# Kernel tuning notes

Measured on AMD Instinct MI355X. Metric: run time of the kernel, lower is better.

## Reference

```python
import jax, jax.numpy as jnp
import numpy as np

B, S, D = 1, 65536, 1024
NH = 8
HD = D // NH
M = 8          # memory_tokens
HID = 2048     # d_model * mlp_ratio(2.0)
EPS_LN = 1e-5
EPS_L = 1e-9


def setup_inputs() -> dict:
    key = jax.random.key(0)
    ks = jax.random.split(key, 16)
    def w(k, shape, s=0.02):
        return jax.random.normal(k, shape, dtype=jnp.float32) * s
    return {
        "h_img_seq": jax.random.normal(ks[0], (B, S, D), dtype=jnp.float32),
        "latents": w(ks[1], (M, D)),
        "wq": w(ks[2], (D, D)), "bq": jnp.zeros((D,), jnp.float32),
        "wk": w(ks[3], (D, D)), "bk": jnp.zeros((D,), jnp.float32),
        "wv": w(ks[4], (D, D)), "bv": jnp.zeros((D,), jnp.float32),
        "wo": w(ks[5], (D, D)), "bo": jnp.zeros((D,), jnp.float32),
        "ln_g": jnp.ones((D,), jnp.float32), "ln_b": jnp.zeros((D,), jnp.float32),
        "w1": w(ks[6], (D, HID)), "b1": jnp.zeros((HID,), jnp.float32),
        "w2": w(ks[7], (HID, D)), "b2": jnp.zeros((D,), jnp.float32),
    }


def reference(h_img_seq, latents, wq, bq, wk, bk, wv, bv, wo, bo,
              ln_g, ln_b, w1, b1, w2, b2):
    b, s, d = h_img_seq.shape
    scale = HD ** -0.5
    # queries from latents: [M, NH, HD] (shared across batch)
    q = (latents @ wq + bq).reshape(M, NH, HD).astype(jnp.float32)
    # K/V projections over the long sequence: [B, S, NH, HD] (fp32 accum)
    k = (h_img_seq @ wk + bk).reshape(b, s, NH, HD).astype(jnp.float32)
    v = (h_img_seq @ wv + bv).reshape(b, s, NH, HD).astype(jnp.float32)
    # online-softmax over chunks == stable softmax over full S (denominator l + 1e-9)
    logits = jnp.einsum('mhd,bshd->bhms', q, k) * scale          # [B, NH, M, S]
    mmax = jnp.max(logits, axis=-1, keepdims=True)
    e = jnp.exp(logits - mmax)
    l = jnp.sum(e, axis=-1, keepdims=True)                       # [B, NH, M, 1]
    acc = jnp.einsum('bhms,bshd->bhmd', e, v)                    # [B, NH, M, HD]
    out = acc / (l + EPS_L)
    out = out.transpose(0, 2, 1, 3).reshape(b, M, d).astype(h_img_seq.dtype)
    out = out @ wo + bo
    # MLP: LayerNorm -> Linear -> GELU(exact) -> Linear, residual
    mu = jnp.mean(out, axis=-1, keepdims=True)
    var = jnp.mean((out - mu) ** 2, axis=-1, keepdims=True)
    h = (out - mu) * jax.lax.rsqrt(var + EPS_LN) * ln_g + ln_b
    h = jax.nn.gelu(h @ w1 + b1, approximate=False) @ w2 + b2
    out = out + h
    m_vec = out.mean(axis=1)
    return (out, m_vec)
```

## Files before the change

### kernel.cpp

```cpp
#include <hip/hip_runtime.h>
#include <stdint.h>
#include <math.h>

#define S_LEN   65536
#define DM      1024
#define HD_     128
#define HID_    2048
#define SCALE_F 0.08838834764831845f

typedef float          f32x4  __attribute__((ext_vector_type(4)));
typedef short          bf16x8 __attribute__((ext_vector_type(8)));
typedef unsigned short u16;

__device__ __forceinline__ u16 f2bf(float f) {
  union { float f; uint32_t u; } v; v.f = f;
  uint32_t u = v.u;
  u += 0x7FFFu + ((u >> 16) & 1u);
  return (u16)(u >> 16);
}

__device__ __forceinline__ bf16x8 pack_bf8(const float* f) {
  union { bf16x8 v; u16 s[8]; } r;
#pragma unroll
  for (int i = 0; i < 8; ++i) r.s[i] = f2bf(f[i]);
  return r.v;
}

#define WS_Q      0u
#define WS_QKA    32768u
#define WS_QBK    163840u
#define WS_LSUM   164352u
#define WS_PLSUM  164608u
#define WS_XN     167936u
#define WS_EWH    430080u
#define WS_PMAX   698368u
#define WS_OATT   960512u
#define WS_O2     993280u
#define WS_H1     1026048u
#define WS_PBASE  2097152u
#define WS_LOGITS 2097152u
#define WS_PEW    2097152u
#define WS_E      34603008u

template<int KS>
__global__ __launch_bounds__(256) void k_sk8(const float* __restrict__ X,
                                             const float* __restrict__ W,
                                             float* __restrict__ P,
                                             int C, int K, int ncg) {
  int cg = blockIdx.x % ncg, kb = blockIdx.x / ncg;
  int c = (cg << 9) + threadIdx.x * 2;
  int k0 = kb * KS;
  float2 acc[8];
#pragma unroll
  for (int r = 0; r < 8; ++r) { acc[r].x = 0.f; acc[r].y = 0.f; }
  const float* wp = W + (size_t)k0 * C + c;
#pragma unroll 8
  for (int i = 0; i < KS; ++i) {
    float2 w = *(const float2*)wp; wp += C;
#pragma unroll
    for (int r = 0; r < 8; ++r) {
      float xv = X[r * K + k0 + i];
      acc[r].x += xv * w.x; acc[r].y += xv * w.y;
    }
  }
  float* pp = P + (size_t)(kb * 8) * C + c;
#pragma unroll
  for (int r = 0; r < 8; ++r) *(float2*)(pp + (size_t)r * C) = acc[r];
}

__global__ __launch_bounds__(256) void k_sk8h(const float* __restrict__ ewh,
                                              const float* __restrict__ wv,
                                              float* __restrict__ Pa) {
  int h = blockIdx.x & 7, kb = blockIdx.x >> 3;
  int lane = threadIdx.x & 63, q4 = threadIdx.x >> 6;
  int c = h * 128 + lane * 2;
  int k0 = kb * 64 + q4 * 16;
  const float* xp = ewh + h * 8192 + k0 * 8;
  const float* wp = wv + (size_t)k0 * 1024 + c;
  float2 acc[8];
#pragma unroll
  for (int m = 0; m < 8; ++m) { acc[m].x = 0.f; acc[m].y = 0.f; }
#pragma unroll
  for (int i = 0; i < 16; ++i) {
    float2 w = *(const float2*)wp; wp += 1024;
#pragma unroll
    for (int m = 0; m < 8; ++m) {
      float xv = xp[i * 8 + m];
      acc[m].x += xv * w.x; acc[m].y += xv * w.y;
    }
  }
  int slab = kb * 4 + q4;
  float* pp = Pa + (size_t)(slab * 8) * 1024 + c;
#pragma unroll
  for (int m = 0; m < 8; ++m) *(float2*)(pp + (size_t)m * 1024) = acc[m];
}

__global__ void k_red_q(const float* __restrict__ P, const float* __restrict__ bq,
                        float* __restrict__ q) {
  int idx = blockIdx.x * 256 + threadIdx.x;
  int m = idx >> 10, c = idx & 1023;
  float s = bq[c];
#pragma unroll 8
  for (int ks = 0; ks < 32; ++ks) s += P[(size_t)(ks * 8 + m) * 1024 + c];
  q[idx] = s;
}

__global__ __launch_bounds__(256) void k_foldqk(const float* __restrict__ q,
                                                const float* __restrict__ wk,
                                                const float* __restrict__ bk,
                                                u16* __restrict__ qka,
                                                float* __restrict__ qbk) {
  __shared__ float tile[64 * 129];
  int h = blockIdx.x & 7, ib = blockIdx.x >> 3;
  int i0 = ib * 64;
  int t = threadIdx.x;
  if (ib == 0 && t < 64) {
    int m = t >> 3, part = t & 7;
    float s = 0.f;
#pragma unroll
    for (int d = 0; d < 16; ++d)
      s += q[m * 1024 + h * 128 + part * 16 + d] * bk[h * 128 + part * 16 + d];
    s += __shfl_xor(s, 1);
    s += __shfl_xor(s, 2);
    s += __shfl_xor(s, 4);
    if (part == 0) qbk[m * 8 + h] = s * SCALE_F;
  }
  {
    int ii = t >> 2, dg = (t & 3) * 32;
    const float* src = wk + (size_t)(i0 + ii) * 1024 + h * 128 + dg;
    float* dst = tile + ii * 129 + dg;
#pragma unroll
    for (int u = 0; u < 8; ++u) {
      f32x4 v = *(const f32x4*)(src + u * 4);
      dst[u * 4 + 0] = v[0]; dst[u * 4 + 1] = v[1];
      dst[u * 4 + 2] = v[2]; dst[u * 4 + 3] = v[3];
    }
  }
  __syncthreads();
  int ii = t & 63, q4 = t >> 6;
  int i = i0 + ii;
  float a0 = 0.f, a1 = 0.f;
#pragma unroll 16
  for (int d = 0; d < 128; ++d) {
    float w = tile[ii * 129 + d];
    a0 += q[(q4 * 2 + 0) * 1024 + h * 128 + d] * w;
    a1 += q[(q4 * 2 + 1) * 1024 + h * 128 + d] * w;
  }
#pragma unroll
  for (int j = 0; j < 2; ++j) {
    int m = q4 * 2 + j;
    int r = m * 8 + h;
    float val = (j == 0 ? a0 : a1) * SCALE_F;
    int K0 = i >> 5, rb = r >> 4, hi = (i & 31) >> 3, e = i & 7, l16 = r & 15;
    int lane = hi * 16 + l16;
    qka[(((K0 * 4 + rb) * 64 + lane) << 3) + e] = f2bf(val);
  }
}

__global__ __launch_bounds__(256) void k_logits(
    const float* __restrict__ h, const u16* __restrict__ qka,
    const float* __restrict__ qbk, float* __restrict__ logits,
    float* __restrict__ pmax) {
  __shared__ float pmL[4 * 64];
  int t = threadIdx.x, wg = blockIdx.x;
  int w = t >> 6, l = t & 63;
  int g = l >> 4, l15 = l & 15;
  int scol = wg * 64 + w * 16 + l15;
  const bf16x8* qf = (const bf16x8*)qka;

  f32x4 acc[4];
#pragma unroll
  for (int rb = 0; rb < 4; ++rb) acc[rb] = (f32x4){0.f, 0.f, 0.f, 0.f};

#pragma unroll 2
  for (int ks = 0; ks < 32; ++ks) {
    const float* hp = h + (size_t)scol * DM + ks * 32 + g * 8;
    float fb[8];
    f32x4 f0 = *(const f32x4*)hp;
    f32x4 f1 = *(const f32x4*)(hp + 4);
    fb[0]=f0[0]; fb[1]=f0[1]; fb[2]=f0[2]; fb[3]=f0[3];
    fb[4]=f1[0]; fb[5]=f1[1]; fb[6]=f1[2]; fb[7]=f1[3];
    bf16x8 bfr = pack_bf8(fb);
#pragma unroll
    for (int rb = 0; rb < 4; ++rb) {
      bf16x8 af = qf[(ks * 4 + rb) * 64 + l];
      acc[rb] = __builtin_amdgcn_mfma_f32_16x16x32_bf16(af, bfr, acc[rb], 0, 0, 0);
    }
  }

#pragma unroll
  for (int rb = 0; rb < 4; ++rb) {
#pragma unroll
    for (int j = 0; j < 4; ++j) {
      int r = rb * 16 + g * 4 + j;
      float val = acc[rb][j] + qbk[r];
      logits[(size_t)r * S_LEN + scol] = val;
      float mx = val;
      mx = fmaxf(mx, __shfl_xor(mx, 1));
      mx = fmaxf(mx, __shfl_xor(mx, 2));
      mx = fmaxf(mx, __shfl_xor(mx, 4));
      mx = fmaxf(mx, __shfl_xor(mx, 8));
      if (l15 == 0) pmL[w * 64 + r] = mx;
    }
  }
  __syncthreads();
  if (t < 64) {
    float m0 = fmaxf(fmaxf(pmL[t], pmL[64 + t]), fmaxf(pmL[128 + t], pmL[192 + t]));
    pmax[(size_t)t * 1024 + wg] = m0;
  }
}

__global__ void k_make_e(const float* __restrict__ logits, const float* __restrict__ pmax,
                         u16* __restrict__ E, float* __restrict__ plsum) {
  int b = blockIdx.x, t = threadIdx.x;
  int r = b >> 3, sc = b & 7;
  __shared__ float red[256];
  float mv = -3.0e38f;
#pragma unroll
  for (int i = 0; i < 4; ++i) mv = fmaxf(mv, pmax[(size_t)r * 1024 + t + i * 256]);
  red[t] = mv; __syncthreads();
  for (int s = 128; s > 0; s >>= 1) {
    if (t < s) red[t] = fmaxf(red[t], red[t + s]);
    __syncthreads();
  }
  float gm = red[0];
  __syncthreads();

  size_t base = (size_t)r * S_LEN + sc * 8192 + t * 32;
  const float* lp = logits + base;
  u16* ep = E + base;
  float sum = 0.f;
#pragma unroll
  for (int gi = 0; gi < 4; ++gi) {
    f32x4 f0 = *(const f32x4*)(lp + gi * 8);
    f32x4 f1 = *(const f32x4*)(lp + gi * 8 + 4);
    float e[8];
#pragma unroll
    for (int i = 0; i < 4; ++i) { e[i] = expf(f0[i] - gm); e[4 + i] = expf(f1[i] - gm); }
    union { uint4 u4; u16 s[8]; } pk;
#pragma unroll
    for (int i = 0; i < 8; ++i) { sum += e[i]; pk.s[i] = f2bf(e[i]); }
    *(uint4*)(ep + gi * 8) = pk.u4;
  }
  red[t] = sum; __syncthreads();
  for (int s = 128; s > 0; s >>= 1) {
    if (t < s) red[t] += red[t + s];
    __syncthreads();
  }
  if (t == 0) plsum[r * 8 + sc] = red[0];
}

__global__ __launch_bounds__(256) void k_pass2(
    const float* __restrict__ h, const u16* __restrict__ E, float* __restrict__ pew) {
  int t = threadIdx.x;
  int chunk = blockIdx.x >> 3, ctile = blockIdx.x & 7;
  int w = t >> 6, l = t & 63;
  int g = l >> 4, l15 = l & 15;
  int c0 = ctile * 128 + w * 32;
  f32x4 acc[4][2];
#pragma unroll
  for (int rb = 0; rb < 4; ++rb)
#pragma unroll
    for (int cb = 0; cb < 2; ++cb) acc[rb][cb] = (f32x4){0.f, 0.f, 0.f, 0.f};

  int kbase = chunk * 1024;
#pragma unroll 2
  for (int ks = 0; ks < 32; ++ks) {
    int k0 = kbase + ks * 32;
    bf16x8 af[4];
#pragma unroll
    for (int rb = 0; rb < 4; ++rb) {
      size_t eidx = (size_t)(rb * 16 + l15) * S_LEN + k0 + g * 8;
      uint4 u = *(const uint4*)(E + eidx);
      af[rb] = *(bf16x8*)&u;
    }
    bf16x8 bfb[2];
#pragma unroll
    for (int cb = 0; cb < 2; ++cb) {
      const float* hp = h + (size_t)(k0 + g * 8) * DM + c0 + cb * 16 + l15;
      float fb[8];
#pragma unroll
      for (int e = 0; e < 8; ++e) fb[e] = hp[(size_t)e * DM];
      bfb[cb] = pack_bf8(fb);
    }
#pragma unroll
    for (int rb = 0; rb < 4; ++rb)
#pragma unroll
      for (int cb = 0; cb < 2; ++cb)
        acc[rb][cb] = __builtin_amdgcn_mfma_f32_16x16x32_bf16(af[rb], bfb[cb], acc[rb][cb], 0, 0, 0);
  }
  float* pw = pew + (size_t)chunk * 65536;
#pragma unroll
  for (int rb = 0; rb < 4; ++rb)
#pragma unroll
    for (int cb = 0; cb < 2; ++cb)
#pragma unroll
      for (int j = 0; j < 4; ++j) {
        int r = rb * 16 + g * 4 + j;
        int c = c0 + cb * 16 + l15;
        pw[(size_t)r * 1024 + c] = acc[rb][cb][j];
      }
}

__global__ void k_red_ew(const float* __restrict__ pew, float* __restrict__ ewh,
                         const float* __restrict__ plsum, float* __restrict__ lsum) {
  int idx = blockIdx.x * 256 + threadIdx.x;
  const float* p = pew + idx;
  float s = 0.f;
#pragma unroll 8
  for (int ch = 0; ch < 64; ++ch) s += p[(size_t)ch * 65536];
  int r = idx >> 10, c = idx & 1023;
  int m = r >> 3, hh = r & 7;
  ewh[hh * 8192 + c * 8 + m] = s;
  if (blockIdx.x == 0 && threadIdx.x < 64) {
    float lv = 0.f;
#pragma unroll
    for (int i = 0; i < 8; ++i) lv += plsum[threadIdx.x * 8 + i];
    lsum[threadIdx.x] = lv;
  }
}

__global__ void k_red_attn(const float* __restrict__ Pa, const float* __restrict__ lsum,
                           const float* __restrict__ bv, float* __restrict__ oatt) {
  int idx = blockIdx.x * 256 + threadIdx.x;
  int m = idx >> 10, col = idx & 1023;
  int r = m * 8 + (col >> 7);
  float s = 0.f;
#pragma unroll 8
  for (int ks = 0; ks < 64; ++ks) s += Pa[(size_t)(ks * 8 + m) * 1024 + col];
  float lv = lsum[r];
  oatt[idx] = (s + lv * bv[col]) / (lv + 1e-9f);
}

__global__ void k_red_o2_ln(const float* __restrict__ P, const float* __restrict__ bo,
                            const float* __restrict__ g, const float* __restrict__ b,
                            float* __restrict__ o2, float* __restrict__ xn) {
  int m = blockIdx.x, t = threadIdx.x;
  __shared__ float red[256], red2[256];
  f32x4 s4 = ((const f32x4*)bo)[t];
#pragma unroll 8
  for (int ks = 0; ks < 32; ++ks) {
    f32x4 p = ((const f32x4*)(P + (size_t)(ks * 8 + m) * 1024))[t];
#pragma unroll
    for (int j = 0; j < 4; ++j) s4[j] += p[j];
  }
  ((f32x4*)(o2 + m * 1024))[t] = s4;
  float s = s4[0] + s4[1] + s4[2] + s4[3];
  float s2 = s4[0]*s4[0] + s4[1]*s4[1] + s4[2]*s4[2] + s4[3]*s4[3];
  red[t] = s; red2[t] = s2; __syncthreads();
  for (int st = 128; st > 0; st >>= 1) {
    if (t < st) { red[t] += red[t + st]; red2[t] += red2[t + st]; }
    __syncthreads();
  }
  float mu = red[0] * (1.f / DM);
  float var = fmaxf(red2[0] * (1.f / DM) - mu * mu, 0.f);
  float rstd = rsqrtf(var + 1e-5f);
  f32x4 gg = ((const f32x4*)g)[t];
  f32x4 bb = ((const f32x4*)b)[t];
  f32x4 o;
#pragma unroll
  for (int j = 0; j < 4; ++j) o[j] = (s4[j] - mu) * rstd * gg[j] + bb[j];
  ((f32x4*)(xn + m * 1024))[t] = o;
}

__global__ void k_red_h1(const float* __restrict__ P, const float* __restrict__ b1,
                         float* __restrict__ h1) {
  int idx = blockIdx.x * 256 + threadIdx.x;
  int m = idx >> 11, j = idx & 2047;
  float s = b1[j];
#pragma unroll 8
  for (int ks = 0; ks < 32; ++ks) s += P[(size_t)(ks * 8 + m) * 2048 + j];
  h1[idx] = 0.5f * s * (1.f + erff(s * 0.70710678118654752f));
}

__global__ void k_red_out_mvec(const float* __restrict__ P, const float* __restrict__ b2,
                               const float* __restrict__ o2, float* __restrict__ out) {
  int idx = blockIdx.x * 256 + threadIdx.x;
  int j = idx >> 3, m = idx & 7;
  float s = b2[j];
#pragma unroll 8
  for (int ks = 0; ks < 64; ++ks) s += P[(size_t)(ks * 8 + m) * 1024 + j];
  s += o2[m * 1024 + j];
  out[m * 1024 + j] = s;
  float sm = s;
  sm += __shfl_xor(sm, 1);
  sm += __shfl_xor(sm, 2);
  sm += __shfl_xor(sm, 4);
  if (m == 0) out[8192 + j] = sm * 0.125f;
}

extern "C" void kernel_launch(void* const* d_in, const int* in_sizes, int n_in,
                              void* d_out, int out_size, void* d_ws, size_t ws_size,
                              hipStream_t stream) {
  (void)in_sizes; (void)n_in; (void)out_size; (void)ws_size;
  const float* h   = (const float*)d_in[0];
  const float* lat = (const float*)d_in[1];
  const float* wq  = (const float*)d_in[2];
  const float* bq  = (const float*)d_in[3];
  const float* wk  = (const float*)d_in[4];
  const float* bk  = (const float*)d_in[5];
  const float* wv  = (const float*)d_in[6];
  const float* bv  = (const float*)d_in[7];
  const float* wo  = (const float*)d_in[8];
  const float* bo  = (const float*)d_in[9];
  const float* lng = (const float*)d_in[10];
  const float* lnb = (const float*)d_in[11];
  const float* w1  = (const float*)d_in[12];
  const float* b1  = (const float*)d_in[13];
  const float* w2  = (const float*)d_in[14];
  const float* b2  = (const float*)d_in[15];
  float* out = (float*)d_out;
  char* ws = (char*)d_ws;

  float* q      = (float*)(ws + WS_Q);
  u16*   qka    = (u16*)  (ws + WS_QKA);
  float* qbk    = (float*)(ws + WS_QBK);
  float* lsum   = (float*)(ws + WS_LSUM);
  float* plsum  = (float*)(ws + WS_PLSUM);
  float* xn     = (float*)(ws + WS_XN);
  float* ewh    = (float*)(ws + WS_EWH);
  float* pmax   = (float*)(ws + WS_PMAX);
  float* oatt   = (float*)(ws + WS_OATT);
  float* o2     = (float*)(ws + WS_O2);
  float* h1     = (float*)(ws + WS_H1);
  float* P      = (float*)(ws + WS_PBASE);
  float* logits = (float*)(ws + WS_LOGITS);
  float* pew    = (float*)(ws + WS_PEW);
  u16*   E      = (u16*)  (ws + WS_E);

  hipLaunchKernelGGL((k_sk8<32>), dim3(64),  dim3(256), 0, stream, lat, wq, P, 1024, 1024, 2);
  hipLaunchKernelGGL(k_red_q,     dim3(32),  dim3(256), 0, stream, P, bq, q);
  hipLaunchKernelGGL(k_foldqk,    dim3(128), dim3(256), 0, stream, q, wk, bk, qka, qbk);
  hipLaunchKernelGGL(k_logits,    dim3(1024), dim3(256), 0, stream, h, qka, qbk, logits, pmax);
  hipLaunchKernelGGL(k_make_e,    dim3(512), dim3(256), 0, stream, logits, pmax, E, plsum);
  hipLaunchKernelGGL(k_pass2,     dim3(512), dim3(256), 0, stream, h, E, pew);
  hipLaunchKernelGGL(k_red_ew,    dim3(256), dim3(256), 0, stream, pew, ewh, plsum, lsum);
  hipLaunchKernelGGL(k_sk8h,      dim3(128), dim3(256), 0, stream, ewh, wv, P);
  hipLaunchKernelGGL(k_red_attn,  dim3(32),  dim3(256), 0, stream, P, lsum, bv, oatt);
  hipLaunchKernelGGL((k_sk8<32>), dim3(64),  dim3(256), 0, stream, oatt, wo, P, 1024, 1024, 2);
  hipLaunchKernelGGL(k_red_o2_ln, dim3(8),   dim3(256), 0, stream, P, bo, lng, lnb, o2, xn);
  hipLaunchKernelGGL((k_sk8<32>), dim3(128), dim3(256), 0, stream, xn, w1, P, 2048, 1024, 4);
  hipLaunchKernelGGL(k_red_h1,    dim3(64),  dim3(256), 0, stream, P, b1, h1);
  hipLaunchKernelGGL((k_sk8<32>), dim3(128), dim3(256), 0, stream, h1, w2, P, 1024, 2048, 2);
  hipLaunchKernelGGL(k_red_out_mvec, dim3(32), dim3(256), 0, stream, P, b2, o2, out);
}
```

Baseline: 563.4 us.

## Fuse logits, exp and E·h accumulation into one attention kernel

Replaces the four-kernel pipeline (logits, global-max and exp, E·h pass, reduction) with one kernel. Each block handles 256 sequence rows. It computes q·k logits with MFMA, exponentiates them in shared memory and immediately accumulates E·h, while the h tile is still likely in cache. This avoids writing and re-reading the fp32 logits and bf16 E buffers and one full stream of h, and it drops the global-max pass by exponentiating raw logits. The costs are overflow risk when logits are large, a larger per-block partial buffer that the finish kernel must reduce, and only one 1024-thread block per CU.

```diff
diff --git a/kernel.cpp b/kernel.cpp
--- a/kernel.cpp
+++ b/kernel.cpp
@@ -30,17 +30,14 @@
 #define WS_QKA    32768u
 #define WS_QBK    163840u
 #define WS_LSUM   164352u
-#define WS_PLSUM  164608u
 #define WS_XN     167936u
 #define WS_EWH    430080u
-#define WS_PMAX   698368u
 #define WS_OATT   960512u
 #define WS_O2     993280u
 #define WS_H1     1026048u
+#define WS_PLSUMB 1179648u
 #define WS_PBASE  2097152u
-#define WS_LOGITS 2097152u
-#define WS_PEW    2097152u
-#define WS_E      34603008u
+#define WS_POUT   2097152u
 
 template<int KS>
 __global__ __launch_bounds__(256) void k_sk8(const float* __restrict__ X,
@@ -157,165 +154,119 @@
   }
 }
 
-__global__ __launch_bounds__(256) void k_logits(
+__global__ __launch_bounds__(1024, 4) void k_attn(
     const float* __restrict__ h, const u16* __restrict__ qka,
-    const float* __restrict__ qbk, float* __restrict__ logits,
-    float* __restrict__ pmax) {
-  __shared__ float pmL[4 * 64];
-  int t = threadIdx.x, wg = blockIdx.x;
+    const float* __restrict__ qbk, float* __restrict__ pout,
+    float* __restrict__ plsumb) {
+  __shared__ float Lred[16][64][16];
+  __shared__ u16 Efrag[4 * 64 * 8];
+  int t = threadIdx.x, blk = blockIdx.x;
   int w = t >> 6, l = t & 63;
-  int g = l >> 4, l15 = l & 15;
-  int scol = wg * 64 + w * 16 + l15;
+  int l15 = l & 15, g = l >> 4;
+  int stile = w & 1, kslice = w >> 1;
+  int sr = t >> 4, sp = t & 15;
+  float lreg = 0.f;
+  int cbase = w * 64;
+  f32x4 acc[4][4];
+#pragma unroll
+  for (int i = 0; i < 4; ++i)
+#pragma unroll
+    for (int j2 = 0; j2 < 4; ++j2) acc[i][j2] = (f32x4){0.f, 0.f, 0.f, 0.f};
   const bf16x8* qf = (const bf16x8*)qka;
-
-  f32x4 acc[4];
-#pragma unroll
-  for (int rb = 0; rb < 4; ++rb) acc[rb] = (f32x4){0.f, 0.f, 0.f, 0.f};
-
-#pragma unroll 2
-  for (int ks = 0; ks < 32; ++ks) {
-    const float* hp = h + (size_t)scol * DM + ks * 32 + g * 8;
-    float fb[8];
-    f32x4 f0 = *(const f32x4*)hp;
-    f32x4 f1 = *(const f32x4*)(hp + 4);
-    fb[0]=f0[0]; fb[1]=f0[1]; fb[2]=f0[2]; fb[3]=f0[3];
-    fb[4]=f1[0]; fb[5]=f1[1]; fb[6]=f1[2]; fb[7]=f1[3];
-    bf16x8 bfr = pack_bf8(fb);
-#pragma unroll
-    for (int rb = 0; rb < 4; ++rb) {
-      bf16x8 af = qf[(ks * 4 + rb) * 64 + l];
-      acc[rb] = __builtin_amdgcn_mfma_f32_16x16x32_bf16(af, bfr, acc[rb], 0, 0, 0);
-    }
-  }
-
-#pragma unroll
-  for (int rb = 0; rb < 4; ++rb) {
-#pragma unroll
-    for (int j = 0; j < 4; ++j) {
-      int r = rb * 16 + g * 4 + j;
-      float val = acc[rb][j] + qbk[r];
-      logits[(size_t)r * S_LEN + scol] = val;
-      float mx = val;
-      mx = fmaxf(mx, __shfl_xor(mx, 1));
-      mx = fmaxf(mx, __shfl_xor(mx, 2));
-      mx = fmaxf(mx, __shfl_xor(mx, 4));
-      mx = fmaxf(mx, __shfl_xor(mx, 8));
-      if (l15 == 0) pmL[w * 64 + r] = mx;
-    }
-  }
+  float qb = qbk[sr];
+
+  for (int st = 0; st < 8; ++st) {
+    int s0row = blk * 256 + st * 32;
+    f32x4 a2[4];
+#pragma unroll
+    for (int rb = 0; rb < 4; ++rb) a2[rb] = (f32x4){0.f, 0.f, 0.f, 0.f};
+    const float* hrow = h + (size_t)(s0row + stile * 16 + l15) * DM;
+#pragma unroll
+    for (int kk = 0; kk < 4; ++kk) {
+      int k0 = kslice * 128 + kk * 32;
+      const float* hp = hrow + k0 + g * 8;
+      f32x4 f0 = *(const f32x4*)hp;
+      f32x4 f1 = *(const f32x4*)(hp + 4);
+      float fb[8] = {f0[0], f0[1], f0[2], f0[3], f1[0], f1[1], f1[2], f1[3]};
+      bf16x8 bfr = pack_bf8(fb);
+      int K0 = k0 >> 5;
+#pragma unroll
+      for (int rb = 0; rb < 4; ++rb)
+        a2[rb] = __builtin_amdgcn_mfma_f32_16x16x32_bf16(qf[(K0 * 4 + rb) * 64 + l], bfr, a2[rb], 0, 0, 0);
+    }
+#pragma unroll
+    for (int rb = 0; rb < 4; ++rb)
+#pragma unroll
+      for (int j = 0; j < 4; ++j)
+        Lred[w][rb * 16 + g * 4 + j][l15] = a2[rb][j];
+    __syncthreads();
+    {
+      int s0 = 2 * sp;
+      int wsel = s0 >> 4;
+      float L0 = qb, L1 = qb;
+#pragma unroll
+      for (int ks = 0; ks < 8; ++ks) {
+        L0 += Lred[ks * 2 + wsel][sr][s0 & 15];
+        L1 += Lred[ks * 2 + wsel][sr][(s0 + 1) & 15];
+      }
+      float E0 = expf(L0), E1 = expf(L1);
+      lreg += E0 + E1;
+      int rt = sr >> 4;
+      int lp = (s0 >> 3) * 16 + (sr & 15);
+      uint32_t pk2 = (uint32_t)f2bf(E0) | ((uint32_t)f2bf(E1) << 16);
+      *(uint32_t*)(Efrag + rt * 512 + lp * 8 + (s0 & 7)) = pk2;
+    }
+    __syncthreads();
+#pragma unroll
+    for (int ct = 0; ct < 4; ++ct) {
+      int c = cbase + ct * 16 + l15;
+      const float* hp2 = h + (size_t)(s0row + g * 8) * DM + c;
+      float fb2[8];
+#pragma unroll
+      for (int e = 0; e < 8; ++e) fb2[e] = hp2[(size_t)e * DM];
+      bf16x8 bfb = pack_bf8(fb2);
+#pragma unroll
+      for (int rt = 0; rt < 4; ++rt) {
+        bf16x8 ef = *(const bf16x8*)(Efrag + rt * 512 + l * 8);
+        acc[rt][ct] = __builtin_amdgcn_mfma_f32_16x16x32_bf16(ef, bfb, acc[rt][ct], 0, 0, 0);
+      }
+    }
+    __syncthreads();
+  }
+  float* pb = pout + (size_t)blk * 65536;
+#pragma unroll
+  for (int rt = 0; rt < 4; ++rt)
+#pragma unroll
+    for (int ct = 0; ct < 4; ++ct)
+#pragma unroll
+      for (int j = 0; j < 4; ++j) {
+        int r = rt * 16 + g * 4 + j;
+        int c = cbase + ct * 16 + l15;
+        pb[r * 1024 + c] = acc[rt][ct][j];
+      }
+  ((float*)Lred)[t] = lreg;
   __syncthreads();
   if (t < 64) {
-    float m0 = fmaxf(fmaxf(pmL[t], pmL[64 + t]), fmaxf(pmL[128 + t], pmL[192 + t]));
-    pmax[(size_t)t * 1024 + wg] = m0;
-  }
-}
-
-__global__ void k_make_e(const float* __restrict__ logits, const float* __restrict__ pmax,
-                         u16* __restrict__ E, float* __restrict__ plsum) {
-  int b = blockIdx.x, t = threadIdx.x;
-  int r = b >> 3, sc = b & 7;
-  __shared__ float red[256];
-  float mv = -3.0e38f;
-#pragma unroll
-  for (int i = 0; i < 4; ++i) mv = fmaxf(mv, pmax[(size_t)r * 1024 + t + i * 256]);
-  red[t] = mv; __syncthreads();
-  for (int s = 128; s > 0; s >>= 1) {
-    if (t < s) red[t] = fmaxf(red[t], red[t + s]);
-    __syncthreads();
-  }
-  float gm = red[0];
-  __syncthreads();
-
-  size_t base = (size_t)r * S_LEN + sc * 8192 + t * 32;
-  const float* lp = logits + base;
-  u16* ep = E + base;
-  float sum = 0.f;
-#pragma unroll
-  for (int gi = 0; gi < 4; ++gi) {
-    f32x4 f0 = *(const f32x4*)(lp + gi * 8);
-    f32x4 f1 = *(const f32x4*)(lp + gi * 8 + 4);
-    float e[8];
-#pragma unroll
-    for (int i = 0; i < 4; ++i) { e[i] = expf(f0[i] - gm); e[4 + i] = expf(f1[i] - gm); }
-    union { uint4 u4; u16 s[8]; } pk;
-#pragma unroll
-    for (int i = 0; i < 8; ++i) { sum += e[i]; pk.s[i] = f2bf(e[i]); }
-    *(uint4*)(ep + gi * 8) = pk.u4;
-  }
-  red[t] = sum; __syncthreads();
-  for (int s = 128; s > 0; s >>= 1) {
-    if (t < s) red[t] += red[t + s];
-    __syncthreads();
-  }
-  if (t == 0) plsum[r * 8 + sc] = red[0];
-}
-
-__global__ __launch_bounds__(256) void k_pass2(
-    const float* __restrict__ h, const u16* __restrict__ E, float* __restrict__ pew) {
-  int t = threadIdx.x;
-  int chunk = blockIdx.x >> 3, ctile = blockIdx.x & 7;
-  int w = t >> 6, l = t & 63;
-  int g = l >> 4, l15 = l & 15;
-  int c0 = ctile * 128 + w * 32;
-  f32x4 acc[4][2];
-#pragma unroll
-  for (int rb = 0; rb < 4; ++rb)
-#pragma unroll
-    for (int cb = 0; cb < 2; ++cb) acc[rb][cb] = (f32x4){0.f, 0.f, 0.f, 0.f};
-
-  int kbase = chunk * 1024;
-#pragma unroll 2
-  for (int ks = 0; ks < 32; ++ks) {
-    int k0 = kbase + ks * 32;
-    bf16x8 af[4];
-#pragma unroll
-    for (int rb = 0; rb < 4; ++rb) {
-      size_t eidx = (size_t)(rb * 16 + l15) * S_LEN + k0 + g * 8;
-      uint4 u = *(const uint4*)(E + eidx);
-      af[rb] = *(bf16x8*)&u;
-    }
-    bf16x8 bfb[2];
-#pragma unroll
-    for (int cb = 0; cb < 2; ++cb) {
-      const float* hp = h + (size_t)(k0 + g * 8) * DM + c0 + cb * 16 + l15;
-      float fb[8];
-#pragma unroll
-      for (int e = 0; e < 8; ++e) fb[e] = hp[(size_t)e * DM];
-      bfb[cb] = pack_bf8(fb);
-    }
-#pragma unroll
-    for (int rb = 0; rb < 4; ++rb)
-#pragma unroll
-      for (int cb = 0; cb < 2; ++cb)
-        acc[rb][cb] = __builtin_amdgcn_mfma_f32_16x16x32_bf16(af[rb], bfb[cb], acc[rb][cb], 0, 0, 0);
-  }
-  float* pw = pew + (size_t)chunk * 65536;
-#pragma unroll
-  for (int rb = 0; rb < 4; ++rb)
-#pragma unroll
-    for (int cb = 0; cb < 2; ++cb)
-#pragma unroll
-      for (int j = 0; j < 4; ++j) {
-        int r = rb * 16 + g * 4 + j;
-        int c = c0 + cb * 16 + l15;
-        pw[(size_t)r * 1024 + c] = acc[rb][cb][j];
-      }
-}
-
-__global__ void k_red_ew(const float* __restrict__ pew, float* __restrict__ ewh,
-                         const float* __restrict__ plsum, float* __restrict__ lsum) {
-  int idx = blockIdx.x * 256 + threadIdx.x;
-  const float* p = pew + idx;
+    float s = 0.f;
+#pragma unroll
+    for (int i = 0; i < 16; ++i) s += ((float*)Lred)[t * 16 + i];
+    plsumb[blk * 64 + t] = s;
+  }
+}
+
+__global__ void k_finish(const float* __restrict__ pout, const float* __restrict__ plsumb,
+                         float* __restrict__ ewh, float* __restrict__ lsum) {
+  int idx = blockIdx.x * 1024 + threadIdx.x;
   float s = 0.f;
-#pragma unroll 8
-  for (int ch = 0; ch < 64; ++ch) s += p[(size_t)ch * 65536];
+  const float* p = pout + idx;
+#pragma unroll 8
+  for (int b = 0; b < 256; ++b) s += p[(size_t)b * 65536];
   int r = idx >> 10, c = idx & 1023;
-  int m = r >> 3, hh = r & 7;
-  ewh[hh * 8192 + c * 8 + m] = s;
+  ewh[(r & 7) * 8192 + c * 8 + (r >> 3)] = s;
   if (blockIdx.x == 0 && threadIdx.x < 64) {
     float lv = 0.f;
-#pragma unroll
-    for (int i = 0; i < 8; ++i) lv += plsum[threadIdx.x * 8 + i];
+#pragma unroll 8
+    for (int b = 0; b < 256; ++b) lv += plsumb[b * 64 + threadIdx.x];
     lsum[threadIdx.x] = lv;
   }
 }
@@ -416,25 +367,20 @@
   u16*   qka    = (u16*)  (ws + WS_QKA);
   float* qbk    = (float*)(ws + WS_QBK);
   float* lsum   = (float*)(ws + WS_LSUM);
-  float* plsum  = (float*)(ws + WS_PLSUM);
   float* xn     = (float*)(ws + WS_XN);
   float* ewh    = (float*)(ws + WS_EWH);
-  float* pmax   = (float*)(ws + WS_PMAX);
   float* oatt   = (float*)(ws + WS_OATT);
   float* o2     = (float*)(ws + WS_O2);
   float* h1     = (float*)(ws + WS_H1);
+  float* plsumb = (float*)(ws + WS_PLSUMB);
   float* P      = (float*)(ws + WS_PBASE);
-  float* logits = (float*)(ws + WS_LOGITS);
-  float* pew    = (float*)(ws + WS_PEW);
-  u16*   E      = (u16*)  (ws + WS_E);
+  float* pout   = (float*)(ws + WS_POUT);
 
   hipLaunchKernelGGL((k_sk8<32>), dim3(64),  dim3(256), 0, stream, lat, wq, P, 1024, 1024, 2);
   hipLaunchKernelGGL(k_red_q,     dim3(32),  dim3(256), 0, stream, P, bq, q);
   hipLaunchKernelGGL(k_foldqk,    dim3(128), dim3(256), 0, stream, q, wk, bk, qka, qbk);
-  hipLaunchKernelGGL(k_logits,    dim3(1024), dim3(256), 0, stream, h, qka, qbk, logits, pmax);
-  hipLaunchKernelGGL(k_make_e,    dim3(512), dim3(256), 0, stream, logits, pmax, E, plsum);
-  hipLaunchKernelGGL(k_pass2,     dim3(512), dim3(256), 0, stream, h, E, pew);
-  hipLaunchKernelGGL(k_red_ew,    dim3(256), dim3(256), 0, stream, pew, ewh, plsum, lsum);
+  hipLaunchKernelGGL(k_attn,      dim3(256), dim3(1024), 0, stream, h, qka, qbk, pout, plsumb);
+  hipLaunchKernelGGL(k_finish,    dim3(64),  dim3(1024), 0, stream, pout, plsumb, ewh, lsum);
   hipLaunchKernelGGL(k_sk8h,      dim3(128), dim3(256), 0, stream, ewh, wv, P);
   hipLaunchKernelGGL(k_red_attn,  dim3(32),  dim3(256), 0, stream, P, lsum, bv, oatt);
   hipLaunchKernelGGL((k_sk8<32>), dim3(64),  dim3(256), 0, stream, oatt, wo, P, 1024, 1024, 2);
```

New measurement: 603.4 us. +7.1%, slower.
